# Performance work log

Measured on AMD Instinct MI355X. Metric: run time of the kernel, lower is better.

The kernel has to match this reference:

```python
import jax, jax.numpy as jnp
import numpy as np

B, S, D = 2, 1024, 1024
N_HEADS = 16
R = 128
M = 8
N_NEURONS = 256


def group_gate(gate, n_basis):
    # gate: [B,S,N] -> [B,S,M], sum over consecutive groups, then normalize
    b, s, n = gate.shape
    gs = n // n_basis  # exact by construction (256/8)
    g = gate.reshape(b, s, n_basis, gs).sum(axis=-1)
    return g / (g.sum(axis=-1, keepdims=True) + 1e-8)


def feature_fn(x, neurons, weights):
    # x:[B,S,D], neurons:[M,D,R], weights:[B,S,M] -> h:[B,S,R]
    all_h = jnp.einsum('bsd,mdr->bsmr', x, neurons)
    return jnp.einsum('bsmr,bsm->bsr', all_h, weights)


def restore_fn(h, neurons, weights):
    # h:[B,S,R], neurons:[M,R,D], weights:[B,S,M] -> [B,S,D]
    pre = jnp.einsum('bsr,bsm->bsmr', h, weights)
    return jnp.einsum('bsmr,mrd->bsd', pre, neurons)


def setup_inputs() -> dict:
    key = jax.random.key(0)
    ks = jax.random.split(key, 9)
    sc = 0.02
    return {
        'x': jax.random.normal(ks[0], (B, S, D), jnp.float32),
        'qk_f': jax.random.normal(ks[1], (M, D, R), jnp.float32) * sc,
        'qk_r': jax.random.normal(ks[2], (M, R, D), jnp.float32) * sc,
        'v_f': jax.random.normal(ks[3], (M, D, R), jnp.float32) * sc,
        'v_r': jax.random.normal(ks[4], (M, R, D), jnp.float32) * sc,
        'Wg_q': jax.random.normal(ks[5], (D, N_NEURONS), jnp.float32) * sc,
        'Wg_k': jax.random.normal(ks[6], (D, N_NEURONS), jnp.float32) * sc,
        'Wg_v': jax.random.normal(ks[7], (D, N_NEURONS), jnp.float32) * sc,
        'W_O': jax.random.normal(ks[8], (D, D), jnp.float32) * sc,
    }


def reference(x, qk_f, qk_r, v_f, v_r, Wg_q, Wg_k, Wg_v, W_O):
    # Router gates (softmax over neuron dim), then grouped per basis
    g_Q = jax.nn.softmax(jnp.einsum('bsd,dn->bsn', x, Wg_q), axis=-1)
    g_K = jax.nn.softmax(jnp.einsum('bsd,dn->bsn', x, Wg_k), axis=-1)
    g_V = jax.nn.softmax(jnp.einsum('bsd,dn->bsn', x, Wg_v), axis=-1)
    gQ_b = group_gate(g_Q, M)
    gK_b = group_gate(g_K, M)
    gV_b = group_gate(g_V, M)

    Q = restore_fn(feature_fn(x, qk_f, gQ_b), qk_r, gQ_b)
    K = restore_fn(feature_fn(x, qk_f, gK_b), qk_r, gK_b)
    V = restore_fn(feature_fn(x, v_f, gV_b), v_r, gV_b)

    d_head = D // N_HEADS
    Q = Q.reshape(B, S, N_HEADS, d_head).transpose(0, 2, 1, 3)
    K = K.reshape(B, S, N_HEADS, d_head).transpose(0, 2, 1, 3)
    V = V.reshape(B, S, N_HEADS, d_head).transpose(0, 2, 1, 3)

    scale = jnp.sqrt(jnp.float32(d_head))
    scores = jnp.einsum('bhsd,bhtd->bhst', Q, K) / scale
    causal = jnp.tril(jnp.ones((S, S), dtype=jnp.bool_))
    scores = jnp.where(causal, scores, jnp.finfo(scores.dtype).min)
    attn_w = jax.nn.softmax(scores, axis=-1)
    out = jnp.einsum('bhst,bhtd->bhsd', attn_w, V)
    out = out.transpose(0, 2, 1, 3).reshape(B, S, D)
    out = jnp.einsum('bsd,de->bse', out, W_O)
    return out
```

## Files before the change

### kernel.cpp

```cpp
#include <hip/hip_runtime.h>
#include <hip/hip_bf16.h>

#define BB 2
#define SS 1024
#define DD 1024
#define NH 16
#define DH 64
#define MM 8
#define RR 128
#define NN 256
#define NT (BB*SS)

using bf16 = __hip_bfloat16;

typedef __attribute__((ext_vector_type(8))) short short8;
typedef __attribute__((ext_vector_type(4))) short short4v;
typedef __attribute__((ext_vector_type(4))) float f32x4;

__device__ __forceinline__ void stf(float* p, size_t i, float v) { p[i] = v; }
__device__ __forceinline__ void stf(bf16* p, size_t i, float v) { p[i] = __float2bfloat16(v); }

#define GLD16(g, l) __builtin_amdgcn_global_load_lds( \
    (const __attribute__((address_space(1))) void*)(g), \
    (__attribute__((address_space(3))) void*)(l), 16, 0, 0)

__device__ __forceinline__ short8 lds_load8(const short* p) {
    short4v a = *(const short4v*)p;
    short4v b = *(const short4v*)(p + 4);
    short8 r;
    r[0] = a[0]; r[1] = a[1]; r[2] = a[2]; r[3] = a[3];
    r[4] = b[0]; r[5] = b[1]; r[6] = b[2]; r[7] = b[3];
    return r;
}

template <typename TC>
__device__ __forceinline__ void gemm64_body(
    const bf16* __restrict__ A, const bf16* __restrict__ Bt, TC* __restrict__ C,
    int Kdim, int Nz, int m0, int n0, bf16* As, bf16* Bs) {
    const int tid = threadIdx.x;
    const int wave = tid >> 6, lane = tid & 63;
    const int quad = lane >> 4, l15 = lane & 15;
    const int wr = wave >> 1, wc = wave & 1;

    f32x4 acc[2][4];
#pragma unroll
    for (int i = 0; i < 2; ++i)
#pragma unroll
        for (int j = 0; j < 4; ++j) acc[i][j] = (f32x4)0.f;

    for (int k0 = 0; k0 < Kdim; k0 += 64) {
        __syncthreads();
#pragma unroll
        for (int i = 0; i < 2; ++i) {
            const int L = i * 256 + wave * 64 + lane;
            const int row = L >> 3;
            const int gch = (L & 7) ^ ((row >> 1) & 7);
            GLD16(A + (size_t)(m0 + row) * Kdim + k0 + gch * 8, &As[(i * 256 + wave * 64) * 8]);
        }
#pragma unroll
        for (int i = 0; i < 4; ++i) {
            const int L = i * 256 + wave * 64 + lane;
            const int row = L >> 3;
            const int gch = (L & 7) ^ ((row >> 1) & 7);
            GLD16(Bt + (size_t)(n0 + row) * Kdim + k0 + gch * 8, &Bs[(i * 256 + wave * 64) * 8]);
        }
        __syncthreads();

#pragma unroll
        for (int kk = 0; kk < 2; ++kk) {
            short8 aF[2], bF[4];
#pragma unroll
            for (int bi = 0; bi < 2; ++bi) {
                int m = wr * 32 + bi * 16 + l15;
                int slot = (kk * 4 + quad) ^ ((m >> 1) & 7);
                aF[bi] = *(const short8*)&As[(m * 8 + slot) * 8];
            }
#pragma unroll
            for (int bj = 0; bj < 4; ++bj) {
                int n = wc * 64 + bj * 16 + l15;
                int slot = (kk * 4 + quad) ^ ((n >> 1) & 7);
                bF[bj] = *(const short8*)&Bs[(n * 8 + slot) * 8];
            }
#pragma unroll
            for (int bi = 0; bi < 2; ++bi)
#pragma unroll
                for (int bj = 0; bj < 4; ++bj)
                    acc[bi][bj] = __builtin_amdgcn_mfma_f32_16x16x32_bf16(aF[bi], bF[bj], acc[bi][bj], 0, 0, 0);
        }
    }

#pragma unroll
    for (int bi = 0; bi < 2; ++bi)
#pragma unroll
        for (int bj = 0; bj < 4; ++bj)
#pragma unroll
            for (int r = 0; r < 4; ++r) {
                int row = m0 + wr * 32 + bi * 16 + quad * 4 + r;
                int col = n0 + wc * 64 + bj * 16 + l15;
                stf(C, (size_t)row * Nz + col, acc[bi][bj][r]);
            }
}

struct GemmZ {
    const bf16* A[5];
    const bf16* Bt[5];
    void* C[5];
    int N[5];
};

__global__ __launch_bounds__(256) void mfma_proj(GemmZ P, int Kdim) {
    __shared__ bf16 As[64 * 64];
    __shared__ bf16 Bs[128 * 64];
    const int bidx = blockIdx.x;
    int z, xx, yy;
    if (bidx < 512) { z = bidx >> 8; int r = bidx & 255; yy = r >> 3; xx = r & 7; }
    else { int r = bidx - 512; z = 2 + r / 64; r = r % 64; yy = r >> 1; xx = r & 1; }
    gemm64_body<bf16>(P.A[z], P.Bt[z], (bf16*)P.C[z], Kdim, P.N[z], yy * 64, xx * 128, As, Bs);
}

__global__ __launch_bounds__(256) void mfma_restore(GemmZ P, int Kdim) {
    __shared__ bf16 As[64 * 64];
    __shared__ bf16 Bs[128 * 64];
    const int z = blockIdx.z;
    gemm64_body<bf16>(P.A[z], P.Bt[z], (bf16*)P.C[z], Kdim, P.N[z],
                      blockIdx.y * 64, blockIdx.x * 128, As, Bs);
}

__global__ __launch_bounds__(256) void mfma_gemm_64(
    const bf16* __restrict__ A, const bf16* __restrict__ Bt, float* __restrict__ C,
    int Kdim, int Ndim) {
    __shared__ bf16 As[64 * 64];
    __shared__ bf16 Bs[128 * 64];
    gemm64_body<float>(A, Bt, C, Kdim, Ndim, blockIdx.y * 64, blockIdx.x * 128, As, Bs);
}

struct ConvJobs {
    const float* src[9];
    bf16* dst[9];
    int K[9], R[9], G[9];
    int tEnd[9];
};

__global__ void convert_kernel(ConvJobs J) {
    __shared__ float tile[32][33];
    const int b = blockIdx.x;
    int j = 0;
    while (j < 8 && b >= J.tEnd[j]) ++j;
    const int local = b - (j > 0 ? J.tEnd[j - 1] : 0);
    const float* src = J.src[j];
    bf16* dst = J.dst[j];
    const int tid = threadIdx.x;

    if (J.G[j] == 0) {
        size_t base = (size_t)local * 4096 + (size_t)tid * 16;
        const float4* s4 = (const float4*)(src + base);
        short* d = (short*)(dst + base);
#pragma unroll
        for (int c = 0; c < 4; ++c) {
            float4 v = s4[c];
            short4v o;
            bf16 t0 = __float2bfloat16(v.x); o[0] = *(short*)&t0;
            bf16 t1 = __float2bfloat16(v.y); o[1] = *(short*)&t1;
            bf16 t2 = __float2bfloat16(v.z); o[2] = *(short*)&t2;
            bf16 t3 = __float2bfloat16(v.w); o[3] = *(short*)&t3;
            *(short4v*)(d + c * 4) = o;
        }
    } else {
        const int Kj = J.K[j], Rj = J.R[j];
        const int Rb = Rj >> 5, Kb = Kj >> 5;
        const int perG = Kb * Rb;
        const int g = local / perG;
        const int rem = local - g * perG;
        const int kb = rem / Rb, rb = rem - kb * Rb;
        const int tx = tid & 31, ty0 = tid >> 5;
        const float* s = src + ((size_t)(g * Kj + kb * 32) * Rj) + rb * 32 + tx;
#pragma unroll
        for (int p = 0; p < 4; ++p)
            tile[ty0 + p * 8][tx] = s[(size_t)(ty0 + p * 8) * Rj];
        __syncthreads();
        bf16* dd = dst + ((size_t)(g * Rj + rb * 32) * Kj) + kb * 32 + tx;
#pragma unroll
        for (int p = 0; p < 4; ++p)
            dd[(size_t)(ty0 + p * 8) * Kj] = __float2bfloat16(tile[tx][ty0 + p * 8]);
    }
}

__global__ void gate_combine(const bf16* __restrict__ logitsAll,
                             const bf16* __restrict__ allh,
                             bf16* __restrict__ preQ, bf16* __restrict__ preK,
                             bf16* __restrict__ preV) {
    const int t = blockIdx.x;
    const int n = threadIdx.x;
    const int wave = n >> 6, lane = n & 63;
    __shared__ float wred[3][4];
    __shared__ float sred[3][4];
    __shared__ float gred[3][8];

    float v[3], e[3];
#pragma unroll
    for (int z = 0; z < 3; ++z)
        v[z] = __bfloat162float(logitsAll[(size_t)z * NT * NN + (size_t)t * NN + n]);

    float mz[3];
#pragma unroll
    for (int z = 0; z < 3; ++z) {
        mz[z] = v[z];
#pragma unroll
        for (int off = 1; off <= 32; off <<= 1)
            mz[z] = fmaxf(mz[z], __shfl_xor(mz[z], off));
    }
    if (lane == 0) {
#pragma unroll
        for (int z = 0; z < 3; ++z) wred[z][wave] = mz[z];
    }
    __syncthreads();
    float gmax[3];
#pragma unroll
    for (int z = 0; z < 3; ++z)
        gmax[z] = fmaxf(fmaxf(wred[z][0], wred[z][1]), fmaxf(wred[z][2], wred[z][3]));

    float ws[3];
#pragma unroll
    for (int z = 0; z < 3; ++z) {
        e[z] = __expf(v[z] - gmax[z]);
        ws[z] = e[z];
#pragma unroll
        for (int off = 1; off <= 32; off <<= 1)
            ws[z] += __shfl_xor(ws[z], off);
    }
    if (lane == 0) {
#pragma unroll
        for (int z = 0; z < 3; ++z) sred[z][wave] = ws[z];
    }
    float gs[3];
#pragma unroll
    for (int z = 0; z < 3; ++z) {
        gs[z] = e[z];
#pragma unroll
        for (int off = 1; off <= 16; off <<= 1)
            gs[z] += __shfl_xor(gs[z], off);
    }
    __syncthreads();
    float total[3];
#pragma unroll
    for (int z = 0; z < 3; ++z)
        total[z] = sred[z][0] + sred[z][1] + sred[z][2] + sred[z][3];
    if ((n & 31) == 0) {
#pragma unroll
        for (int z = 0; z < 3; ++z) gred[z][n >> 5] = gs[z] / total[z];
    }
    __syncthreads();

    float gv[3][8];
#pragma unroll
    for (int z = 0; z < 3; ++z) {
        float tot = 0.f;
#pragma unroll
        for (int m = 0; m < 8; ++m) tot += gred[z][m];
        float inv = 1.0f / (tot + 1e-8f);
#pragma unroll
        for (int m = 0; m < 8; ++m) gv[z][m] = gred[z][m] * inv;
    }

    const int r0 = n & 127;
    const int half = n >> 7;
    const bf16* src_qk = allh + (size_t)t * 1024;
    const bf16* src_v  = allh + (size_t)NT * DD + (size_t)t * 1024;
    float hq = 0.f, hk = 0.f, hv = 0.f;
#pragma unroll
    for (int m = 0; m < 8; ++m) {
        float aqk = __bfloat162float(src_qk[m * 128 + r0]);
        float av  = __bfloat162float(src_v[m * 128 + r0]);
        hq += aqk * gv[0][m];
        hk += aqk * gv[1][m];
        hv += av  * gv[2][m];
    }
    __syncthreads();
#pragma unroll
    for (int mm = 0; mm < 4; ++mm) {
        int m = half * 4 + mm;
        size_t o = (size_t)t * 1024 + m * 128 + r0;
        preQ[o] = __float2bfloat16(hq * gv[0][m]);
        preK[o] = __float2bfloat16(hk * gv[1][m]);
        preV[o] = __float2bfloat16(hv * gv[2][m]);
    }
}

#define LDK 68

__global__ __launch_bounds__(256) void flash_attn_split(
    const bf16* __restrict__ Q, const bf16* __restrict__ K,
    const bf16* __restrict__ V, float* __restrict__ Opart,
    float* __restrict__ ml) {
    const int bx = blockIdx.x;
    const int c = bx & 511;
    const int second = bx >> 9;
    const int qt = second ? (c >> 5) : (15 - (c >> 5));
    const int half = second;
    const int bh = c & 31;
    const int b = bh >> 4;
    const int h = bh & 15;
    const int h0 = (qt + 2) >> 1;
    const int kt_lo = half ? h0 : 0;
    const int kt_hi = half ? (qt + 1) : h0;

    const int tid = threadIdx.x;
    const int wave = tid >> 6;
    const int lane = tid & 63;
    const int quad = lane >> 4;
    const int l15 = lane & 15;

    __shared__ short Ks[2][64 * 64];
    __shared__ short Vt[2][64 * LDK];
    __shared__ short Ps[4 * 16 * LDK];

    const int q_row = qt * 64 + wave * 16 + l15;
    const bf16* qptr = Q + (size_t)(b * SS + q_row) * DD + h * DH + quad * 8;
    short8 aq0 = *(const short8*)qptr;
    short8 aq1 = *(const short8*)(qptr + 32);

    const int krp = tid & 31;
    const int dhb = (tid >> 5) * 8;

    float m_r[4], l_r[4];
    f32x4 o[4];
#pragma unroll
    for (int r = 0; r < 4; ++r) { m_r[r] = -3.0e38f; l_r[r] = 0.f; }
#pragma unroll
    for (int cc = 0; cc < 4; ++cc) o[cc] = (f32x4)0.f;

    const float scale = 0.125f;

    if (kt_lo < kt_hi) {
#pragma unroll
        for (int i = 0; i < 2; ++i) {
            const int L = i * 256 + wave * 64 + lane;
            const int row = L >> 3;
            const int gch = (L & 7) ^ ((row >> 1) & 7);
            GLD16(K + (size_t)(b * SS + kt_lo * 64 + row) * DD + h * DH + gch * 8,
                  &Ks[0][(i * 256 + wave * 64) * 8]);
        }
        const bf16* s0 = V + (size_t)(b * SS + kt_lo * 64 + 2 * krp) * DD + h * DH + dhb;
        short8 r0 = *(const short8*)s0;
        short8 r1 = *(const short8*)(s0 + DD);
#pragma unroll
        for (int i = 0; i < 8; ++i) {
            unsigned int pk = (unsigned short)r0[i] | ((unsigned int)(unsigned short)r1[i] << 16);
            *(unsigned int*)&Vt[0][(dhb + i) * LDK + 2 * krp] = pk;
        }
        __syncthreads();
    }

    for (int kt = kt_lo; kt < kt_hi; ++kt) {
        const int buf = (kt - kt_lo) & 1;
        const bool pf = (kt + 1 < kt_hi);
        short8 pr0, pr1;
        if (pf) {
#pragma unroll
            for (int i = 0; i < 2; ++i) {
                const int L = i * 256 + wave * 64 + lane;
                const int row = L >> 3;
                const int gch = (L & 7) ^ ((row >> 1) & 7);
                GLD16(K + (size_t)(b * SS + (kt + 1) * 64 + row) * DD + h * DH + gch * 8,
                      &Ks[buf ^ 1][(i * 256 + wave * 64) * 8]);
            }
            const bf16* s0 = V + (size_t)(b * SS + (kt + 1) * 64 + 2 * krp) * DD + h * DH + dhb;
            pr0 = *(const short8*)s0;
            pr1 = *(const short8*)(s0 + DD);
        }

        const short* KsB = Ks[buf];
        f32x4 s[4];
#pragma unroll
        for (int cc = 0; cc < 4; ++cc) {
            int n = cc * 16 + l15;
            int sl0 = quad ^ ((n >> 1) & 7);
            int sl1 = (quad + 4) ^ ((n >> 1) & 7);
            short8 bk0 = *(const short8*)&KsB[(n * 8 + sl0) * 8];
            short8 bk1 = *(const short8*)&KsB[(n * 8 + sl1) * 8];
            f32x4 acc = (f32x4)0.f;
            acc = __builtin_amdgcn_mfma_f32_16x16x32_bf16(aq0, bk0, acc, 0, 0, 0);
            acc = __builtin_amdgcn_mfma_f32_16x16x32_bf16(aq1, bk1, acc, 0, 0, 0);
            s[cc] = acc;
        }

        const bool diag = (kt == qt);
#pragma unroll
        for (int cc = 0; cc < 4; ++cc) {
#pragma unroll
            for (int r = 0; r < 4; ++r) {
                float v = s[cc][r] * scale;
                if (diag) {
                    int row_rel = wave * 16 + quad * 4 + r;
                    int col_rel = cc * 16 + l15;
                    if (col_rel > row_rel) v = -3.0e38f;
                }
                s[cc][r] = v;
            }
        }

        float p[4][4];
        float alpha[4];
#pragma unroll
        for (int r = 0; r < 4; ++r) {
            float mx = fmaxf(fmaxf(s[0][r], s[1][r]), fmaxf(s[2][r], s[3][r]));
            mx = fmaxf(mx, __shfl_xor(mx, 1));
            mx = fmaxf(mx, __shfl_xor(mx, 2));
            mx = fmaxf(mx, __shfl_xor(mx, 4));
            mx = fmaxf(mx, __shfl_xor(mx, 8));
            float new_m = fmaxf(m_r[r], mx);
            alpha[r] = __expf(m_r[r] - new_m);
            float rs = 0.f;
#pragma unroll
            for (int cc = 0; cc < 4; ++cc) {
                float e = __expf(s[cc][r] - new_m);
                p[cc][r] = e;
                rs += e;
            }
            rs += __shfl_xor(rs, 1);
            rs += __shfl_xor(rs, 2);
            rs += __shfl_xor(rs, 4);
            rs += __shfl_xor(rs, 8);
            l_r[r] = l_r[r] * alpha[r] + rs;
            m_r[r] = new_m;
        }
#pragma unroll
        for (int cc = 0; cc < 4; ++cc)
#pragma unroll
            for (int r = 0; r < 4; ++r) o[cc][r] *= alpha[r];

        short* pw = &Ps[wave * 16 * LDK];
#pragma unroll
        for (int cc = 0; cc < 4; ++cc)
#pragma unroll
            for (int r = 0; r < 4; ++r) {
                bf16 hb = __float2bfloat16(p[cc][r]);
                pw[(quad * 4 + r) * LDK + cc * 16 + l15] = *(short*)&hb;
            }

        short8 ap0 = lds_load8(&pw[l15 * LDK + quad * 8]);
        short8 ap1 = lds_load8(&pw[l15 * LDK + 32 + quad * 8]);

        const short* VtB = Vt[buf];
#pragma unroll
        for (int cc = 0; cc < 4; ++cc) {
            short8 bv0 = lds_load8(&VtB[(cc * 16 + l15) * LDK + quad * 8]);
            short8 bv1 = lds_load8(&VtB[(cc * 16 + l15) * LDK + 32 + quad * 8]);
            o[cc] = __builtin_amdgcn_mfma_f32_16x16x32_bf16(ap0, bv0, o[cc], 0, 0, 0);
            o[cc] = __builtin_amdgcn_mfma_f32_16x16x32_bf16(ap1, bv1, o[cc], 0, 0, 0);
        }

        if (pf) {
#pragma unroll
            for (int i = 0; i < 8; ++i) {
                unsigned int pk = (unsigned short)pr0[i] | ((unsigned int)(unsigned short)pr1[i] << 16);
                *(unsigned int*)&Vt[buf ^ 1][(dhb + i) * LDK + 2 * krp] = pk;
            }
        }
        __syncthreads();
    }

    const int idx = (half * 32 + bh) * 16 + qt;
    float* ob = Opart + (size_t)idx * 4096;
#pragma unroll
    for (int cc = 0; cc < 4; ++cc)
#pragma unroll
        for (int r = 0; r < 4; ++r) {
            int row = wave * 16 + quad * 4 + r;
            ob[row * 64 + cc * 16 + l15] = o[cc][r];
        }
    if (l15 == 0) {
#pragma unroll
        for (int r = 0; r < 4; ++r) {
            int row = wave * 16 + quad * 4 + r;
            ml[(size_t)idx * 128 + row] = m_r[r];
            ml[(size_t)idx * 128 + 64 + row] = l_r[r];
        }
    }
}

__global__ void attn_combine(const float* __restrict__ Opart,
                             const float* __restrict__ ml,
                             bf16* __restrict__ out) {
    const int bidx = blockIdx.x;
    const int bh = bidx >> 4;
    const int qt = bidx & 15;
    const int b = bh >> 4;
    const int h = bh & 15;
    const int tid = threadIdx.x;
    const int row = tid >> 2;
    const int cg = tid & 3;

    const int p0 = bh * 16 + qt;
    const int p1 = 512 + bh * 16 + qt;
    float m0 = ml[(size_t)p0 * 128 + row], l0 = ml[(size_t)p0 * 128 + 64 + row];
    float m1 = ml[(size_t)p1 * 128 + row], l1 = ml[(size_t)p1 * 128 + 64 + row];
    float ms = fmaxf(m0, m1);
    float w0 = __expf(m0 - ms), w1 = __expf(m1 - ms);
    float inv = 1.0f / (l0 * w0 + l1 * w1);

    const float* o0 = Opart + (size_t)p0 * 4096 + row * 64 + cg * 16;
    const float* o1 = Opart + (size_t)p1 * 4096 + row * 64 + cg * 16;
    short out16[16];
#pragma unroll
    for (int j = 0; j < 16; j += 4) {
        float4 a = *(const float4*)(o0 + j);
        float4 bb = *(const float4*)(o1 + j);
        float v0 = (a.x * w0 + bb.x * w1) * inv;
        float v1 = (a.y * w0 + bb.y * w1) * inv;
        float v2 = (a.z * w0 + bb.z * w1) * inv;
        float v3 = (a.w * w0 + bb.w * w1) * inv;
        bf16 t0 = __float2bfloat16(v0); out16[j] = *(short*)&t0;
        bf16 t1 = __float2bfloat16(v1); out16[j + 1] = *(short*)&t1;
        bf16 t2 = __float2bfloat16(v2); out16[j + 2] = *(short*)&t2;
        bf16 t3 = __float2bfloat16(v3); out16[j + 3] = *(short*)&t3;
    }
    short* dst = (short*)(out + (size_t)(b * SS + qt * 64 + row) * DD + h * DH + cg * 16);
    *(short8*)dst = *(short8*)&out16[0];
    *(short8*)(dst + 8) = *(short8*)&out16[8];
}

extern "C" void kernel_launch(void* const* d_in, const int* in_sizes, int n_in,
                              void* d_out, int out_size, void* d_ws, size_t ws_size,
                              hipStream_t stream) {
    const float* x    = (const float*)d_in[0];
    const float* qk_f = (const float*)d_in[1];
    const float* qk_r = (const float*)d_in[2];
    const float* v_f  = (const float*)d_in[3];
    const float* v_r  = (const float*)d_in[4];
    const float* Wg_q = (const float*)d_in[5];
    const float* Wg_k = (const float*)d_in[6];
    const float* Wg_v = (const float*)d_in[7];
    const float* W_O  = (const float*)d_in[8];

    char* w = (char*)d_ws;
    const size_t MB = 1 << 20;
    bf16* xb     = (bf16*)(w + 0);
    bf16* wg_bt  = (bf16*)(w + 4 * MB);
    bf16* fbt    = (bf16*)(w + (size_t)(5.5 * MB));
    bf16* logits = (bf16*)(w + (size_t)(9.5 * MB));
    bf16* qkr_bt = (bf16*)(w + 16 * MB);
    bf16* vr_bt  = (bf16*)(w + 18 * MB);
    bf16* wo_bt  = (bf16*)(w + 20 * MB);
    bf16* preQ   = (bf16*)(w + 0);
    bf16* preK   = (bf16*)(w + 4 * MB);
    bf16* Kb     = (bf16*)(w + 8 * MB);
    bf16* Vb     = (bf16*)(w + 12 * MB);
    bf16* attnb  = (bf16*)(w + 0);
    float* Opart = (float*)(w + 32 * MB);
    float* mlbuf = (float*)(w + 48 * MB);
    bf16* allh   = (bf16*)d_out;
    bf16* preV   = allh + (size_t)NT * DD;
    bf16* Qb     = (bf16*)d_out;
    float* out   = (float*)d_out;

    ConvJobs J;
    J.src[0] = qk_f; J.dst[0] = fbt;              J.K[0] = 1024; J.R[0] = 128;  J.G[0] = 8;
    J.src[1] = v_f;  J.dst[1] = fbt + 1024*1024;  J.K[1] = 1024; J.R[1] = 128;  J.G[1] = 8;
    J.src[2] = qk_r; J.dst[2] = qkr_bt;           J.K[2] = 1024; J.R[2] = 1024; J.G[2] = 1;
    J.src[3] = v_r;  J.dst[3] = vr_bt;            J.K[3] = 1024; J.R[3] = 1024; J.G[3] = 1;
    J.src[4] = W_O;  J.dst[4] = wo_bt;            J.K[4] = 1024; J.R[4] = 1024; J.G[4] = 1;
    J.src[5] = Wg_q; J.dst[5] = wg_bt;            J.K[5] = 1024; J.R[5] = 256;  J.G[5] = 1;
    J.src[6] = Wg_k; J.dst[6] = wg_bt + 256*1024; J.K[6] = 1024; J.R[6] = 256;  J.G[6] = 1;
    J.src[7] = Wg_v; J.dst[7] = wg_bt + 2*256*1024; J.K[7] = 1024; J.R[7] = 256; J.G[7] = 1;
    J.src[8] = x;    J.dst[8] = xb;               J.K[8] = 0;    J.R[8] = 0;    J.G[8] = 0;
    int tiles[9] = {1024, 1024, 1024, 1024, 1024, 256, 256, 256, 512};
    int cum = 0;
    for (int i = 0; i < 9; ++i) { cum += tiles[i]; J.tEnd[i] = cum; }
    convert_kernel<<<cum, 256, 0, stream>>>(J);

    GemmZ Pp;
    Pp.A[0] = Pp.A[1] = Pp.A[2] = Pp.A[3] = Pp.A[4] = xb;
    Pp.Bt[0] = fbt;             Pp.Bt[1] = fbt + 1024*1024;
    Pp.Bt[2] = wg_bt;           Pp.Bt[3] = wg_bt + 256*1024;  Pp.Bt[4] = wg_bt + 2*256*1024;
    Pp.C[0] = allh;             Pp.C[1] = allh + (size_t)NT * DD;
    Pp.C[2] = logits;           Pp.C[3] = logits + (size_t)NT * NN;
    Pp.C[4] = logits + 2 * (size_t)NT * NN;
    Pp.N[0] = 1024; Pp.N[1] = 1024; Pp.N[2] = 256; Pp.N[3] = 256; Pp.N[4] = 256;
    mfma_proj<<<dim3(704), 256, 0, stream>>>(Pp, DD);

    gate_combine<<<NT, 256, 0, stream>>>(logits, allh, preQ, preK, preV);

    GemmZ Pr;
    Pr.A[0] = preQ; Pr.A[1] = preK; Pr.A[2] = preV;
    Pr.Bt[0] = qkr_bt; Pr.Bt[1] = qkr_bt; Pr.Bt[2] = vr_bt;
    Pr.C[0] = Qb; Pr.C[1] = Kb; Pr.C[2] = Vb;
    Pr.N[0] = Pr.N[1] = Pr.N[2] = 1024;
    Pr.A[3] = Pr.A[4] = nullptr; Pr.Bt[3] = Pr.Bt[4] = nullptr;
    Pr.C[3] = Pr.C[4] = nullptr; Pr.N[3] = Pr.N[4] = 0;
    mfma_restore<<<dim3(8, 32, 3), 256, 0, stream>>>(Pr, DD);

    flash_attn_split<<<dim3(1024), 256, 0, stream>>>(Qb, Kb, Vb, Opart, mlbuf);

    attn_combine<<<dim3(512), 256, 0, stream>>>(Opart, mlbuf, attnb);

    mfma_gemm_64<<<dim3(8, 32), 256, 0, stream>>>(attnb, wo_bt, out, DD, DD);
}
```

Measured before the change: 195.9 us.

## Use 128x128 GEMM tiles, drop flash split-K combine, batch convert tiles

Adds a 128x128-tile MFMA GEMM body with K-step 32 and uses it for the projection and restore GEMMs, halving their block counts and raising data reuse per block. The flash attention kernel no longer splits the key range in two with a separate combine kernel; each block now walks all key tiles up to the diagonal and writes normalized bf16 output directly. The convert kernel processes four tiles per block. In exchange, the larger tiles and the unsplit attention give fewer blocks, so the GPU's many CUs may be less evenly loaded, and the causal-diagonal blocks become longer.

```diff
diff --git a/kernel.cpp b/kernel.cpp
--- a/kernel.cpp
+++ b/kernel.cpp
@@ -34,6 +34,64 @@
 }
 
 template <typename TC>
+__device__ __forceinline__ void gemm128_body(
+    const bf16* __restrict__ A, const bf16* __restrict__ Bt, TC* __restrict__ C,
+    int Kdim, int Nz, int m0, int n0, bf16* As, bf16* Bs) {
+    const int tid = threadIdx.x;
+    const int wave = tid >> 6, lane = tid & 63;
+    const int quad = lane >> 4, l15 = lane & 15;
+    const int wr = wave >> 1, wc = wave & 1;
+
+    f32x4 acc[4][4];
+#pragma unroll
+    for (int i = 0; i < 4; ++i)
+#pragma unroll
+        for (int j = 0; j < 4; ++j) acc[i][j] = (f32x4)0.f;
+
+    for (int k0 = 0; k0 < Kdim; k0 += 32) {
+        __syncthreads();
+#pragma unroll
+        for (int i = 0; i < 2; ++i) {
+            const int L = i * 256 + wave * 64 + lane;
+            const int row = L >> 2;
+            const int gch = (L & 3) ^ ((row >> 1) & 3);
+            const int ldsbase = (i * 256 + wave * 64) * 8;
+            GLD16(A + (size_t)(m0 + row) * Kdim + k0 + gch * 8, &As[ldsbase]);
+            GLD16(Bt + (size_t)(n0 + row) * Kdim + k0 + gch * 8, &Bs[ldsbase]);
+        }
+        __syncthreads();
+
+        short8 aF[4], bF[4];
+#pragma unroll
+        for (int bi = 0; bi < 4; ++bi) {
+            int m = wr * 64 + bi * 16 + l15;
+            aF[bi] = *(const short8*)&As[(m * 4 + (quad ^ ((m >> 1) & 3))) * 8];
+        }
+#pragma unroll
+        for (int bj = 0; bj < 4; ++bj) {
+            int n = wc * 64 + bj * 16 + l15;
+            bF[bj] = *(const short8*)&Bs[(n * 4 + (quad ^ ((n >> 1) & 3))) * 8];
+        }
+#pragma unroll
+        for (int bi = 0; bi < 4; ++bi)
+#pragma unroll
+            for (int bj = 0; bj < 4; ++bj)
+                acc[bi][bj] = __builtin_amdgcn_mfma_f32_16x16x32_bf16(aF[bi], bF[bj], acc[bi][bj], 0, 0, 0);
+    }
+
+#pragma unroll
+    for (int bi = 0; bi < 4; ++bi)
+#pragma unroll
+        for (int bj = 0; bj < 4; ++bj)
+#pragma unroll
+            for (int r = 0; r < 4; ++r) {
+                int row = m0 + wr * 64 + bi * 16 + quad * 4 + r;
+                int col = n0 + wc * 64 + bj * 16 + l15;
+                stf(C, (size_t)row * Nz + col, acc[bi][bj][r]);
+            }
+}
+
+template <typename TC>
 __device__ __forceinline__ void gemm64_body(
     const bf16* __restrict__ A, const bf16* __restrict__ Bt, TC* __restrict__ C,
     int Kdim, int Nz, int m0, int n0, bf16* As, bf16* Bs) {
@@ -109,21 +167,21 @@
 };
 
 __global__ __launch_bounds__(256) void mfma_proj(GemmZ P, int Kdim) {
-    __shared__ bf16 As[64 * 64];
-    __shared__ bf16 Bs[128 * 64];
+    __shared__ bf16 As[128 * 32];
+    __shared__ bf16 Bs[128 * 32];
     const int bidx = blockIdx.x;
     int z, xx, yy;
-    if (bidx < 512) { z = bidx >> 8; int r = bidx & 255; yy = r >> 3; xx = r & 7; }
-    else { int r = bidx - 512; z = 2 + r / 64; r = r % 64; yy = r >> 1; xx = r & 1; }
-    gemm64_body<bf16>(P.A[z], P.Bt[z], (bf16*)P.C[z], Kdim, P.N[z], yy * 64, xx * 128, As, Bs);
+    if (bidx < 256) { z = bidx >> 7; int r = bidx & 127; yy = r >> 3; xx = r & 7; }
+    else { int r = bidx - 256; z = 2 + r / 32; r = r % 32; yy = r >> 1; xx = r & 1; }
+    gemm128_body<bf16>(P.A[z], P.Bt[z], (bf16*)P.C[z], Kdim, P.N[z], yy * 128, xx * 128, As, Bs);
 }
 
 __global__ __launch_bounds__(256) void mfma_restore(GemmZ P, int Kdim) {
-    __shared__ bf16 As[64 * 64];
-    __shared__ bf16 Bs[128 * 64];
+    __shared__ bf16 As[128 * 32];
+    __shared__ bf16 Bs[128 * 32];
     const int z = blockIdx.z;
-    gemm64_body<bf16>(P.A[z], P.Bt[z], (bf16*)P.C[z], Kdim, P.N[z],
-                      blockIdx.y * 64, blockIdx.x * 128, As, Bs);
+    gemm128_body<bf16>(P.A[z], P.Bt[z], (bf16*)P.C[z], Kdim, P.N[z],
+                       blockIdx.y * 128, blockIdx.x * 128, As, Bs);
 }
 
 __global__ __launch_bounds__(256) void mfma_gemm_64(
@@ -141,47 +199,51 @@
     int tEnd[9];
 };
 
-__global__ void convert_kernel(ConvJobs J) {
+__global__ void convert_kernel(ConvJobs J, int nTiles) {
     __shared__ float tile[32][33];
-    const int b = blockIdx.x;
-    int j = 0;
-    while (j < 8 && b >= J.tEnd[j]) ++j;
-    const int local = b - (j > 0 ? J.tEnd[j - 1] : 0);
-    const float* src = J.src[j];
-    bf16* dst = J.dst[j];
     const int tid = threadIdx.x;
-
-    if (J.G[j] == 0) {
-        size_t base = (size_t)local * 4096 + (size_t)tid * 16;
-        const float4* s4 = (const float4*)(src + base);
-        short* d = (short*)(dst + base);
-#pragma unroll
-        for (int c = 0; c < 4; ++c) {
-            float4 v = s4[c];
-            short4v o;
-            bf16 t0 = __float2bfloat16(v.x); o[0] = *(short*)&t0;
-            bf16 t1 = __float2bfloat16(v.y); o[1] = *(short*)&t1;
-            bf16 t2 = __float2bfloat16(v.z); o[2] = *(short*)&t2;
-            bf16 t3 = __float2bfloat16(v.w); o[3] = *(short*)&t3;
-            *(short4v*)(d + c * 4) = o;
-        }
-    } else {
-        const int Kj = J.K[j], Rj = J.R[j];
-        const int Rb = Rj >> 5, Kb = Kj >> 5;
-        const int perG = Kb * Rb;
-        const int g = local / perG;
-        const int rem = local - g * perG;
-        const int kb = rem / Rb, rb = rem - kb * Rb;
-        const int tx = tid & 31, ty0 = tid >> 5;
-        const float* s = src + ((size_t)(g * Kj + kb * 32) * Rj) + rb * 32 + tx;
-#pragma unroll
-        for (int p = 0; p < 4; ++p)
-            tile[ty0 + p * 8][tx] = s[(size_t)(ty0 + p * 8) * Rj];
+    for (int it = 0; it < 4; ++it) {
+        const int b = blockIdx.x * 4 + it;
+        if (b >= nTiles) break;
+        int j = 0;
+        while (j < 8 && b >= J.tEnd[j]) ++j;
+        const int local = b - (j > 0 ? J.tEnd[j - 1] : 0);
+        const float* src = J.src[j];
+        bf16* dst = J.dst[j];
+
+        if (J.G[j] == 0) {
+            size_t base = (size_t)local * 4096 + (size_t)tid * 16;
+            const float4* s4 = (const float4*)(src + base);
+            short* d = (short*)(dst + base);
+#pragma unroll
+            for (int c = 0; c < 4; ++c) {
+                float4 v = s4[c];
+                short4v o;
+                bf16 t0 = __float2bfloat16(v.x); o[0] = *(short*)&t0;
+                bf16 t1 = __float2bfloat16(v.y); o[1] = *(short*)&t1;
+                bf16 t2 = __float2bfloat16(v.z); o[2] = *(short*)&t2;
+                bf16 t3 = __float2bfloat16(v.w); o[3] = *(short*)&t3;
+                *(short4v*)(d + c * 4) = o;
+            }
+        } else {
+            const int Kj = J.K[j], Rj = J.R[j];
+            const int Rb = Rj >> 5, Kb = Kj >> 5;
+            const int perG = Kb * Rb;
+            const int g = local / perG;
+            const int rem = local - g * perG;
+            const int kb = rem / Rb, rb = rem - kb * Rb;
+            const int tx = tid & 31, ty0 = tid >> 5;
+            const float* s = src + ((size_t)(g * Kj + kb * 32) * Rj) + rb * 32 + tx;
+#pragma unroll
+            for (int p = 0; p < 4; ++p)
+                tile[ty0 + p * 8][tx] = s[(size_t)(ty0 + p * 8) * Rj];
+            __syncthreads();
+            bf16* dd = dst + ((size_t)(g * Rj + rb * 32) * Kj) + kb * 32 + tx;
+#pragma unroll
+            for (int p = 0; p < 4; ++p)
+                dd[(size_t)(ty0 + p * 8) * Kj] = __float2bfloat16(tile[tx][ty0 + p * 8]);
+        }
         __syncthreads();
-        bf16* dd = dst + ((size_t)(g * Rj + rb * 32) * Kj) + kb * 32 + tx;
-#pragma unroll
-        for (int p = 0; p < 4; ++p)
-            dd[(size_t)(ty0 + p * 8) * Kj] = __float2bfloat16(tile[tx][ty0 + p * 8]);
     }
 }
 
@@ -288,21 +350,14 @@
 
 #define LDK 68
 
-__global__ __launch_bounds__(256) void flash_attn_split(
+__global__ __launch_bounds__(256) void flash_attn(
     const bf16* __restrict__ Q, const bf16* __restrict__ K,
-    const bf16* __restrict__ V, float* __restrict__ Opart,
-    float* __restrict__ ml) {
+    const bf16* __restrict__ V, bf16* __restrict__ out) {
     const int bx = blockIdx.x;
-    const int c = bx & 511;
-    const int second = bx >> 9;
-    const int qt = second ? (c >> 5) : (15 - (c >> 5));
-    const int half = second;
-    const int bh = c & 31;
+    const int qt = (bx < 256) ? (15 - (bx >> 5)) : ((bx - 256) >> 5);
+    const int bh = bx & 31;
     const int b = bh >> 4;
     const int h = bh & 15;
-    const int h0 = (qt + 2) >> 1;
-    const int kt_lo = half ? h0 : 0;
-    const int kt_hi = half ? (qt + 1) : h0;
 
     const int tid = threadIdx.x;
     const int wave = tid >> 6;
@@ -331,16 +386,16 @@
 
     const float scale = 0.125f;
 
-    if (kt_lo < kt_hi) {
-#pragma unroll
-        for (int i = 0; i < 2; ++i) {
-            const int L = i * 256 + wave * 64 + lane;
-            const int row = L >> 3;
-            const int gch = (L & 7) ^ ((row >> 1) & 7);
-            GLD16(K + (size_t)(b * SS + kt_lo * 64 + row) * DD + h * DH + gch * 8,
-                  &Ks[0][(i * 256 + wave * 64) * 8]);
-        }
-        const bf16* s0 = V + (size_t)(b * SS + kt_lo * 64 + 2 * krp) * DD + h * DH + dhb;
+#pragma unroll
+    for (int i = 0; i < 2; ++i) {
+        const int L = i * 256 + wave * 64 + lane;
+        const int row = L >> 3;
+        const int gch = (L & 7) ^ ((row >> 1) & 7);
+        GLD16(K + (size_t)(b * SS + row) * DD + h * DH + gch * 8,
+              &Ks[0][(i * 256 + wave * 64) * 8]);
+    }
+    {
+        const bf16* s0 = V + (size_t)(b * SS + 2 * krp) * DD + h * DH + dhb;
         short8 r0 = *(const short8*)s0;
         short8 r1 = *(const short8*)(s0 + DD);
 #pragma unroll
@@ -348,12 +403,12 @@
             unsigned int pk = (unsigned short)r0[i] | ((unsigned int)(unsigned short)r1[i] << 16);
             *(unsigned int*)&Vt[0][(dhb + i) * LDK + 2 * krp] = pk;
         }
-        __syncthreads();
-    }
-
-    for (int kt = kt_lo; kt < kt_hi; ++kt) {
-        const int buf = (kt - kt_lo) & 1;
-        const bool pf = (kt + 1 < kt_hi);
+    }
+    __syncthreads();
+
+    for (int kt = 0; kt <= qt; ++kt) {
+        const int buf = kt & 1;
+        const bool pf = (kt < qt);
         short8 pr0, pr1;
         if (pf) {
 #pragma unroll
@@ -460,64 +515,15 @@
         __syncthreads();
     }
 
-    const int idx = (half * 32 + bh) * 16 + qt;
-    float* ob = Opart + (size_t)idx * 4096;
-#pragma unroll
-    for (int cc = 0; cc < 4; ++cc)
+#pragma unroll
+    for (int cc = 0; cc < 4; ++cc) {
 #pragma unroll
         for (int r = 0; r < 4; ++r) {
-            int row = wave * 16 + quad * 4 + r;
-            ob[row * 64 + cc * 16 + l15] = o[cc][r];
-        }
-    if (l15 == 0) {
-#pragma unroll
-        for (int r = 0; r < 4; ++r) {
-            int row = wave * 16 + quad * 4 + r;
-            ml[(size_t)idx * 128 + row] = m_r[r];
-            ml[(size_t)idx * 128 + 64 + row] = l_r[r];
-        }
-    }
-}
-
-__global__ void attn_combine(const float* __restrict__ Opart,
-                             const float* __restrict__ ml,
-                             bf16* __restrict__ out) {
-    const int bidx = blockIdx.x;
-    const int bh = bidx >> 4;
-    const int qt = bidx & 15;
-    const int b = bh >> 4;
-    const int h = bh & 15;
-    const int tid = threadIdx.x;
-    const int row = tid >> 2;
-    const int cg = tid & 3;
-
-    const int p0 = bh * 16 + qt;
-    const int p1 = 512 + bh * 16 + qt;
-    float m0 = ml[(size_t)p0 * 128 + row], l0 = ml[(size_t)p0 * 128 + 64 + row];
-    float m1 = ml[(size_t)p1 * 128 + row], l1 = ml[(size_t)p1 * 128 + 64 + row];
-    float ms = fmaxf(m0, m1);
-    float w0 = __expf(m0 - ms), w1 = __expf(m1 - ms);
-    float inv = 1.0f / (l0 * w0 + l1 * w1);
-
-    const float* o0 = Opart + (size_t)p0 * 4096 + row * 64 + cg * 16;
-    const float* o1 = Opart + (size_t)p1 * 4096 + row * 64 + cg * 16;
-    short out16[16];
-#pragma unroll
-    for (int j = 0; j < 16; j += 4) {
-        float4 a = *(const float4*)(o0 + j);
-        float4 bb = *(const float4*)(o1 + j);
-        float v0 = (a.x * w0 + bb.x * w1) * inv;
-        float v1 = (a.y * w0 + bb.y * w1) * inv;
-        float v2 = (a.z * w0 + bb.z * w1) * inv;
-        float v3 = (a.w * w0 + bb.w * w1) * inv;
-        bf16 t0 = __float2bfloat16(v0); out16[j] = *(short*)&t0;
-        bf16 t1 = __float2bfloat16(v1); out16[j + 1] = *(short*)&t1;
-        bf16 t2 = __float2bfloat16(v2); out16[j + 2] = *(short*)&t2;
-        bf16 t3 = __float2bfloat16(v3); out16[j + 3] = *(short*)&t3;
-    }
-    short* dst = (short*)(out + (size_t)(b * SS + qt * 64 + row) * DD + h * DH + cg * 16);
-    *(short8*)dst = *(short8*)&out16[0];
-    *(short8*)(dst + 8) = *(short8*)&out16[8];
+            int row = qt * 64 + wave * 16 + quad * 4 + r;
+            int col = cc * 16 + l15;
+            out[(size_t)(b * SS + row) * DD + h * DH + col] = __float2bfloat16(o[cc][r] / l_r[r]);
+        }
+    }
 }
 
 extern "C" void kernel_launch(void* const* d_in, const int* in_sizes, int n_in,
@@ -547,8 +553,6 @@
     bf16* Kb     = (bf16*)(w + 8 * MB);
     bf16* Vb     = (bf16*)(w + 12 * MB);
     bf16* attnb  = (bf16*)(w + 0);
-    float* Opart = (float*)(w + 32 * MB);
-    float* mlbuf = (float*)(w + 48 * MB);
     bf16* allh   = (bf16*)d_out;
     bf16* preV   = allh + (size_t)NT * DD;
     bf16* Qb     = (bf16*)d_out;
@@ -567,7 +571,7 @@
     int tiles[9] = {1024, 1024, 1024, 1024, 1024, 256, 256, 256, 512};
     int cum = 0;
     for (int i = 0; i < 9; ++i) { cum += tiles[i]; J.tEnd[i] = cum; }
-    convert_kernel<<<cum, 256, 0, stream>>>(J);
+    convert_kernel<<<(cum + 3) / 4, 256, 0, stream>>>(J, cum);
 
     GemmZ Pp;
     Pp.A[0] = Pp.A[1] = Pp.A[2] = Pp.A[3] = Pp.A[4] = xb;
@@ -577,7 +581,7 @@
     Pp.C[2] = logits;           Pp.C[3] = logits + (size_t)NT * NN;
     Pp.C[4] = logits + 2 * (size_t)NT * NN;
     Pp.N[0] = 1024; Pp.N[1] = 1024; Pp.N[2] = 256; Pp.N[3] = 256; Pp.N[4] = 256;
-    mfma_proj<<<dim3(704), 256, 0, stream>>>(Pp, DD);
+    mfma_proj<<<dim3(352), 256, 0, stream>>>(Pp, DD);
 
     gate_combine<<<NT, 256, 0, stream>>>(logits, allh, preQ, preK, preV);
 
@@ -588,11 +592,9 @@
     Pr.N[0] = Pr.N[1] = Pr.N[2] = 1024;
     Pr.A[3] = Pr.A[4] = nullptr; Pr.Bt[3] = Pr.Bt[4] = nullptr;
     Pr.C[3] = Pr.C[4] = nullptr; Pr.N[3] = Pr.N[4] = 0;
-    mfma_restore<<<dim3(8, 32, 3), 256, 0, stream>>>(Pr, DD);
-
-    flash_attn_split<<<dim3(1024), 256, 0, stream>>>(Qb, Kb, Vb, Opart, mlbuf);
-
-    attn_combine<<<dim3(512), 256, 0, stream>>>(Opart, mlbuf, attnb);
+    mfma_restore<<<dim3(8, 16, 3), 256, 0, stream>>>(Pr, DD);
+
+    flash_attn<<<dim3(512), 256, 0, stream>>>(Qb, Kb, Vb, attnb);
 
     mfma_gemm_64<<<dim3(8, 32), 256, 0, stream>>>(attnb, wo_bt, out, DD, DD);
 }
```

Measured after the change: 215.5 us. 10.0% more time.
